# Optimization experiments

Hardware: AMD Instinct MI355X
Metric: run time of the kernel (lower is better)

Reference implementation:

```python
import jax, jax.numpy as jnp
import numpy as np

L, B, D = 1024, 2, 1024
H, DH = 16, 64
DFF = 4096
MEM = 1024
T = L + MEM
SCALE = 1.0 / DH ** 0.5
EPS = 1e-5


def _ln(x, g, b):
    mu = jnp.mean(x, axis=-1, keepdims=True)
    var = jnp.var(x, axis=-1, keepdims=True)
    return (x - mu) * jax.lax.rsqrt(var + EPS) * g + b


def _rel_shift(x):
    # x: [L, T, B, H] -> TXL relative shift
    Lq, Tk = x.shape[0], x.shape[1]
    xp = jnp.pad(x, ((0, 0), (1, 0), (0, 0), (0, 0)))
    xp = xp.reshape(Tk + 1, Lq, *x.shape[2:])
    return xp[1:].reshape(x.shape)


def setup_inputs() -> dict:
    key = jax.random.key(0)
    ks = jax.random.split(key, 16)
    s = 0.02
    inp = {
        "x": jax.random.normal(ks[0], (L, B, D), jnp.float32),
        "pos_emb": jax.random.normal(ks[1], (T, B, D), jnp.float32),
        "pos_bias_u": jax.random.normal(ks[2], (H, DH), jnp.float32) * s,
        "pos_bias_v": jax.random.normal(ks[3], (H, DH), jnp.float32) * s,
        "memory": jax.random.normal(ks[4], (MEM, B, D), jnp.float32),
        "Wq": jax.random.normal(ks[5], (D, H * DH), jnp.float32) * s,
        "Wkv": jax.random.normal(ks[6], (D, 2 * H * DH), jnp.float32) * s,
        "Wo": jax.random.normal(ks[7], (H * DH, D), jnp.float32) * s,
        "Wrel": jax.random.normal(ks[8], (D, H * DH), jnp.float32) * s,
        "ln1_g": jnp.ones((D,), jnp.float32),
        "ln1_b": jnp.zeros((D,), jnp.float32),
        "W1": jax.random.normal(ks[9], (D, DFF), jnp.float32) * s,
        "b1": jnp.zeros((DFF,), jnp.float32),
        "W2": jax.random.normal(ks[10], (DFF, D), jnp.float32) * s,
        "b2": jnp.zeros((D,), jnp.float32),
        "ln2_g": jnp.ones((D,), jnp.float32),
        "ln2_b": jnp.zeros((D,), jnp.float32),
    }
    # causal mask: key position j disallowed if j > i + MEM
    i = jnp.arange(L)[:, None]
    j = jnp.arange(T)[None, :]
    inp["mask"] = jnp.broadcast_to((j > i + MEM)[:, :, None], (L, T, B))
    return inp


def reference(x, pos_emb, pos_bias_u, pos_bias_v, memory, mask,
              Wq, Wkv, Wo, Wrel, ln1_g, ln1_b, W1, b1, W2, b2, ln2_g, ln2_b):
    # --- LearnableMultiheadSelfAttention, vanilla branch (seq_len==1) ---
    c = jnp.concatenate([memory, x], axis=0)                  # [T,B,D]
    kv = c @ Wkv                                              # [T,B,2*H*DH]
    k, v = jnp.split(kv, 2, axis=-1)
    k = k.reshape(T, B, H, DH)
    v = v.reshape(T, B, H, DH)
    r = (pos_emb @ Wrel).reshape(T, B, H, DH)                 # [T,B,H,DH]
    q = (x @ Wq).reshape(L, B, H, DH)                         # [L,B,H,DH]

    AC = jnp.einsum('ibnd,jbnd->ijbn', q + pos_bias_u, k)     # [L,T,B,H]
    BD = jnp.einsum('ibnd,jbnd->ijbn', q + pos_bias_v, r)
    BD = _rel_shift(BD)

    score = (AC + BD) * SCALE
    score = jnp.where(mask[:, :, :, None], -jnp.inf, score)
    prob = jax.nn.softmax(score, axis=1)                      # softmax over keys (dim 1)
    attn_matrix = prob.mean(axis=(2, 3))                      # [L,T]

    vec = jnp.einsum('ijbn,jbnd->ibnd', prob, v)
    attn_out = vec.reshape(L, B, H * DH) @ Wo
    out = _ln(x + attn_out, ln1_g, ln1_b)

    # --- PositionwiseFF ---
    ff = jax.nn.relu(out @ W1 + b1) @ W2 + b2
    out = _ln(out + ff, ln2_g, ln2_b)
    return out, attn_matrix
```

## Files before the change

### kernel.cpp

```cpp
#include <hip/hip_runtime.h>
#include <hip/hip_bf16.h>
#include <hip/hip_fp16.h>

using bf16 = __hip_bfloat16;

#define LQ      1024
#define NBAT    2
#define DMOD    1024
#define NHEAD   16
#define DHEAD   64
#define DFFN    4096
#define MEMLEN  1024
#define TKEY    2048
#define HDIM    1024
#define SCALE_F 0.125f
#define EPS_F   1e-5f
#define NVTILE  392

typedef __attribute__((ext_vector_type(8))) short short8;
typedef __attribute__((ext_vector_type(4))) float f32x4;

__device__ __forceinline__ float ldf(const float* p) { return *p; }
__device__ __forceinline__ float ldf(const bf16* p) { return __bfloat162float(*p); }
__device__ __forceinline__ void stf(float* p, float v) { *p = v; }
__device__ __forceinline__ void stf(bf16* p, float v) { *p = __float2bfloat16(v); }

__device__ __forceinline__ void cpy4(bf16* dst, const float* src) {
    float4 w = *(const float4*)src;
    bf16 t[4] = {__float2bfloat16(w.x), __float2bfloat16(w.y),
                 __float2bfloat16(w.z), __float2bfloat16(w.w)};
    *(uint2*)dst = *(uint2*)t;
}
__device__ __forceinline__ void cpy4(bf16* dst, const bf16* src) {
    *(uint2*)dst = *(const uint2*)src;
}

__device__ __forceinline__ void gload_lds16(const bf16* g, bf16* l) {
    __builtin_amdgcn_global_load_lds(
        (const __attribute__((address_space(1))) unsigned int*)g,
        (__attribute__((address_space(3))) unsigned int*)l, 16, 0, 0);
}

#define SWZ(row, colE) ((row) * 64 + ((colE) ^ (((row) & 7) << 3)))

__global__ __launch_bounds__(256)
void cvt3_bf16_k(const float* __restrict__ s0, bf16* __restrict__ d0, int n0,
                 const float* __restrict__ s1, bf16* __restrict__ d1, int n1,
                 const float* __restrict__ s2, bf16* __restrict__ d2, int n2)
{
    int i = (blockIdx.x * 256 + threadIdx.x) * 8;
    const float* s; bf16* d;
    if (i < n0)           { s = s0; d = d0; }
    else if (i < n0 + n1) { s = s1; d = d1; i -= n0; }
    else if (i < n0 + n1 + n2) { s = s2; d = d2; i -= n0 + n1; }
    else return;
    float4 v0 = *(const float4*)(s + i);
    float4 v1 = *(const float4*)(s + i + 4);
    bf16 t[8] = {__float2bfloat16(v0.x), __float2bfloat16(v0.y),
                 __float2bfloat16(v0.z), __float2bfloat16(v0.w),
                 __float2bfloat16(v1.x), __float2bfloat16(v1.y),
                 __float2bfloat16(v1.z), __float2bfloat16(v1.w)};
    *(uint4*)(d + i) = *(uint4*)t;
}

__device__ __forceinline__ void tcvt_tile(const float* __restrict__ W,
                                          bf16* __restrict__ Wt,
                                          int K, int N, int n0, int k0, int tid,
                                          bf16 (*tile)[65])
{
    const int r = tid >> 2, cb = (tid & 3) * 16;
    #pragma unroll
    for (int e = 0; e < 16; e++)
        tile[r][cb + e] = __float2bfloat16(W[(size_t)(k0 + r) * N + n0 + cb + e]);
    __syncthreads();
    bf16 t[16];
    #pragma unroll
    for (int e = 0; e < 16; e++) t[e] = tile[cb + e][r];
    bf16* dst = Wt + (size_t)(n0 + r) * K + k0 + cb;
    *(uint4*)dst       = ((uint4*)t)[0];
    *(uint4*)(dst + 8) = ((uint4*)t)[1];
}

__global__ __launch_bounds__(256)
void tcvt_bf16_k(const float* __restrict__ W, bf16* __restrict__ Wt, int K, int N)
{
    __shared__ alignas(16) bf16 tile[64][65];
    tcvt_tile(W, Wt, K, N, blockIdx.x * 64, blockIdx.y * 64, threadIdx.x, tile);
}

__global__ __launch_bounds__(256)
void tcvt3_k(const float* __restrict__ Wkv_, bf16* __restrict__ dkv,
             const float* __restrict__ Wrel_, bf16* __restrict__ dr,
             const float* __restrict__ Wq_, bf16* __restrict__ dq)
{
    __shared__ alignas(16) bf16 tile[64][65];
    int bid = blockIdx.x;
    const float* W; bf16* Wt; int N;
    if (bid < 512)      { W = Wkv_;  Wt = dkv; N = 2048; }
    else if (bid < 768) { W = Wrel_; Wt = dr;  N = 1024; bid -= 512; }
    else                { W = Wq_;   Wt = dq;  N = 1024; bid -= 768; }
    const int nb = N / 64;
    tcvt_tile(W, Wt, DMOD, N, (bid % nb) * 64, (bid / nb) * 64, threadIdx.x, tile);
}

template<int SPLITS, bool RELU, typename TOUT>
__device__ __forceinline__ void gemm128_body(
    const bf16* __restrict__ A, const bf16* __restrict__ Bt,
    const float* __restrict__ bias, TOUT* __restrict__ Cbase,
    int M, int N, int K, int bx, int by, int bz,
    bf16* __restrict__ As, bf16* __restrict__ Bs)
{
    const int tid  = threadIdx.x;
    const int wave = tid >> 6, lane = tid & 63;
    const int m0 = by * 128, n0 = bx * 128;
    const int g = lane >> 4, c16 = lane & 15;
    const int wr = (wave >> 1) * 64, wc = (wave & 1) * 64;

    const int klen   = K / SPLITS;
    const int kstart = bz * klen;
    TOUT* C = Cbase + (size_t)bz * M * N;

    f32x4 acc[4][4];
    #pragma unroll
    for (int mi = 0; mi < 4; mi++)
        #pragma unroll
        for (int ni = 0; ni < 4; ni++) acc[mi][ni] = (f32x4)(0.f);

    const int r0 = (wave << 5) + (lane >> 3);
    const int cc = (((lane & 7) ^ (lane >> 3)) << 3);
    const bf16* agp = A  + (size_t)(m0 + r0) * K + kstart + cc;
    const bf16* bgp = Bt + (size_t)(n0 + r0) * K + kstart + cc;
    const int lb = wave * 2048;

    #pragma unroll
    for (int q = 0; q < 4; q++) {
        gload_lds16(agp + (size_t)(q * 8) * K, As + lb + q * 512);
        gload_lds16(bgp + (size_t)(q * 8) * K, Bs + lb + q * 512);
    }

    int cur = 0;
    for (int k0 = 0; k0 < klen; k0 += 64) {
        if (k0 + 64 < klen) {
            #pragma unroll
            for (int q = 0; q < 4; q++) {
                gload_lds16(agp + k0 + 64 + (size_t)(q * 8) * K,
                            As + (cur ^ 1) * 8192 + lb + q * 512);
                gload_lds16(bgp + k0 + 64 + (size_t)(q * 8) * K,
                            Bs + (cur ^ 1) * 8192 + lb + q * 512);
            }
            asm volatile("s_waitcnt vmcnt(8)" ::: "memory");
        } else {
            asm volatile("s_waitcnt vmcnt(0)" ::: "memory");
        }
        __builtin_amdgcn_s_barrier();
        short8 af[4][2], bfr[4][2];
        #pragma unroll
        for (int mi = 0; mi < 4; mi++) {
            const int row = wr + mi * 16 + c16;
            af[mi][0] = *(const short8*)&As[cur * 8192 + SWZ(row, g * 8)];
            af[mi][1] = *(const short8*)&As[cur * 8192 + SWZ(row, 32 + g * 8)];
        }
        #pragma unroll
        for (int ni = 0; ni < 4; ni++) {
            const int row = wc + ni * 16 + c16;
            bfr[ni][0] = *(const short8*)&Bs[cur * 8192 + SWZ(row, g * 8)];
            bfr[ni][1] = *(const short8*)&Bs[cur * 8192 + SWZ(row, 32 + g * 8)];
        }
        #pragma unroll
        for (int mi = 0; mi < 4; mi++)
            #pragma unroll
            for (int ni = 0; ni < 4; ni++) {
                acc[mi][ni] = __builtin_amdgcn_mfma_f32_16x16x32_bf16(
                                  af[mi][0], bfr[ni][0], acc[mi][ni], 0, 0, 0);
                acc[mi][ni] = __builtin_amdgcn_mfma_f32_16x16x32_bf16(
                                  af[mi][1], bfr[ni][1], acc[mi][ni], 0, 0, 0);
            }
        __builtin_amdgcn_s_barrier();
        cur ^= 1;
    }

    const int crow = g * 4;
    #pragma unroll
    for (int ni = 0; ni < 4; ni++) {
        const int n = n0 + wc + ni * 16 + c16;
        const float bv = (SPLITS == 1 && bias) ? bias[n] : 0.f;
        #pragma unroll
        for (int mi = 0; mi < 4; mi++) {
            #pragma unroll
            for (int reg = 0; reg < 4; reg++) {
                const int m = m0 + wr + mi * 16 + crow + reg;
                float v = acc[mi][ni][reg] + bv;
                if (RELU) v = fmaxf(v, 0.f);
                stf(C + (size_t)m * N + n, v);
            }
        }
    }
}

template<int SPLITS, bool RELU, typename TOUT>
__global__ __launch_bounds__(256)
void mgemm128_k(const bf16* __restrict__ A, const bf16* __restrict__ Bt,
                const float* __restrict__ bias, TOUT* __restrict__ Cbase,
                int M, int N, int K)
{
    __shared__ alignas(16) bf16 As[2 * 128 * 64];
    __shared__ alignas(16) bf16 Bs[2 * 128 * 64];
    gemm128_body<SPLITS, RELU, TOUT>(A, Bt, bias, Cbase, M, N, K,
                                     blockIdx.x, blockIdx.y, blockIdx.z, As, Bs);
}

__global__ __launch_bounds__(256)
void proj3_k(const bf16* __restrict__ catc, const bf16* __restrict__ wkvt,
             bf16* __restrict__ kvb,
             const bf16* __restrict__ posc, const bf16* __restrict__ wrelt,
             bf16* __restrict__ rb,
             const bf16* __restrict__ xb, const bf16* __restrict__ wqt,
             float* __restrict__ qb)
{
    __shared__ alignas(16) bf16 As[2 * 128 * 64];
    __shared__ alignas(16) bf16 Bs[2 * 128 * 64];
    int bid = blockIdx.x;
    if (bid < 512) {
        gemm128_body<1, false, bf16>(catc, wkvt, nullptr, kvb,
                                     TKEY * NBAT, 2 * HDIM, DMOD,
                                     bid & 15, bid >> 4, 0, As, Bs);
    } else if (bid < 768) {
        bid -= 512;
        gemm128_body<1, false, bf16>(posc, wrelt, nullptr, rb,
                                     TKEY * NBAT, HDIM, DMOD,
                                     bid & 7, bid >> 3, 0, As, Bs);
    } else {
        bid -= 768;
        gemm128_body<1, false, float>(xb, wqt, nullptr, qb,
                                      LQ * NBAT, HDIM, DMOD,
                                      bid & 7, bid >> 3, 0, As, Bs);
    }
}

template<typename TA, typename TOUT, bool RELU>
__global__ __launch_bounds__(256)
void mgemm64_k(const TA* __restrict__ A0, const TA* __restrict__ A1, int rowsplit,
               const float* __restrict__ Bw, const float* __restrict__ bias,
               TOUT* __restrict__ C, int M, int N, int K)
{
    __shared__ alignas(16) bf16 As[64][72];
    __shared__ alignas(16) bf16 Bs[64][72];
    const int tid  = threadIdx.x;
    const int m0   = blockIdx.y * 64;
    const int n0   = blockIdx.x * 64;
    const int wave = tid >> 6, lane = tid & 63;
    const int g = lane >> 4, c16 = lane & 15;

    f32x4 acc[4];
    #pragma unroll
    for (int nt = 0; nt < 4; nt++) acc[nt] = (f32x4)(0.f);

    const int ar = tid >> 2, akc = (tid & 3) * 16;
    const int grow = m0 + ar;
    const TA* Arow = (grow < rowsplit) ? (A0 + (size_t)grow * K)
                                       : (A1 + (size_t)(grow - rowsplit) * K);
    const int bn = tid & 63, bkb = (tid >> 6) * 16;
    const float* Bcol = Bw + n0 + bn;

    for (int k0 = 0; k0 < K; k0 += 64) {
        cpy4(&As[ar][akc],      Arow + k0 + akc);
        cpy4(&As[ar][akc + 4],  Arow + k0 + akc + 4);
        cpy4(&As[ar][akc + 8],  Arow + k0 + akc + 8);
        cpy4(&As[ar][akc + 12], Arow + k0 + akc + 12);
        {
            bf16 t16[16];
            #pragma unroll
            for (int e = 0; e < 16; e++)
                t16[e] = __float2bfloat16(Bcol[(size_t)(k0 + bkb + e) * N]);
            *(uint4*)&Bs[bn][bkb]     = *(uint4*)&t16[0];
            *(uint4*)&Bs[bn][bkb + 8] = *(uint4*)&t16[8];
        }
        __syncthreads();
        const short8 a0 = *(const short8*)&As[wave * 16 + c16][g * 8];
        const short8 a1 = *(const short8*)&As[wave * 16 + c16][32 + g * 8];
        #pragma unroll
        for (int nt = 0; nt < 4; nt++) {
            acc[nt] = __builtin_amdgcn_mfma_f32_16x16x32_bf16(
                          a0, *(const short8*)&Bs[nt * 16 + c16][g * 8], acc[nt], 0, 0, 0);
            acc[nt] = __builtin_amdgcn_mfma_f32_16x16x32_bf16(
                          a1, *(const short8*)&Bs[nt * 16 + c16][32 + g * 8], acc[nt], 0, 0, 0);
        }
        __syncthreads();
    }

    const int crow = (lane >> 4) * 4, ccol = lane & 15;
    #pragma unroll
    for (int nt = 0; nt < 4; nt++) {
        const int n = n0 + nt * 16 + ccol;
        const float bv = bias ? bias[n] : 0.f;
        #pragma unroll
        for (int rr = 0; rr < 4; rr++) {
            const int m = m0 + wave * 16 + crow + rr;
            float v = acc[nt][rr] + bv;
            if (RELU) v = fmaxf(v, 0.f);
            stf(C + (size_t)m * N + n, v);
        }
    }
}

union Frag8 { bf16 h[8]; short8 v; };

template<bool WRSC>
__global__ __launch_bounds__(256)
void flash_attn_k(const float* __restrict__ q, const bf16* __restrict__ kv,
                  const bf16* __restrict__ rg, const float* __restrict__ ub,
                  const float* __restrict__ vb,
                  float* __restrict__ m_arr, float* __restrict__ l_arr,
                  bf16* __restrict__ vec, __half* __restrict__ scr)
{
    __shared__ alignas(16) bf16 Ks[64][72];
    __shared__ alignas(16) bf16 Rs[128][72];
    __shared__ alignas(16) bf16 Vt[64][72];
    __shared__ alignas(16) bf16 BDs[64][136];

    const int itile = (blockIdx.y < (NBAT * NHEAD / 2))
                          ? blockIdx.x : (gridDim.x - 1 - blockIdx.x);
    const int i0 = itile * 64;
    const int bh = blockIdx.y;
    const int b = bh >> 4, h = bh & 15;
    const int tid = threadIdx.x;
    const int wave = tid >> 6, lane = tid & 63;
    const int g = lane >> 4, c16 = lane & 15;
    const int dib = wave * 16 + g * 4;
    const int tbase = itile * 17 + itile * (itile - 1) / 2;

    Frag8 fu0, fu1, fv0, fv1;
    {
        const float* qrow = q + ((size_t)(i0 + wave * 16 + c16) * NBAT + b) * HDIM + h * DHEAD;
        const float* ubp = ub + h * DHEAD;
        const float* vbp = vb + h * DHEAD;
        #pragma unroll
        for (int e = 0; e < 8; e++) {
            float q0 = qrow[g * 8 + e], q1 = qrow[32 + g * 8 + e];
            fu0.h[e] = __float2bfloat16(q0 + ubp[g * 8 + e]);
            fu1.h[e] = __float2bfloat16(q1 + ubp[32 + g * 8 + e]);
            fv0.h[e] = __float2bfloat16(q0 + vbp[g * 8 + e]);
            fv1.h[e] = __float2bfloat16(q1 + vbp[32 + g * 8 + e]);
        }
    }

    float mrow[4] = {-3e38f, -3e38f, -3e38f, -3e38f};
    float lrow[4] = {0.f, 0.f, 0.f, 0.f};
    f32x4 Oacc[4];
    #pragma unroll
    for (int nt = 0; nt < 4; nt++) Oacc[nt] = (f32x4)(0.f);

    const int ntiles = i0 / 64 + 17;

    for (int t = 0; t < ntiles; t++) {
        const int j0 = t * 64;
        const int jj0 = j0 + (LQ - 64) - i0;
        __half* scp = nullptr;
        if (WRSC) scp = scr + ((size_t)bh * NVTILE + tbase + t) * 4096;
        {
            const int row = tid >> 2, dbase = (tid & 3) * 16;
            const bf16* src = kv + ((size_t)(j0 + row) * NBAT + b) * (2 * HDIM)
                                 + h * DHEAD + dbase;
            *(uint4*)&Ks[row][dbase]     = *(const uint4*)src;
            *(uint4*)&Ks[row][dbase + 8] = *(const uint4*)(src + 8);
        }
        {
            const int row = tid >> 1, dbase = (tid & 1) * 32;
            const int jj = jj0 + row;
            if (jj < TKEY) {
                const bf16* src = rg + ((size_t)jj * NBAT + b) * HDIM + h * DHEAD + dbase;
                #pragma unroll
                for (int u = 0; u < 4; u++)
                    *(uint4*)&Rs[row][dbase + u * 8] = *(const uint4*)(src + u * 8);
            } else {
                const uint4 z = make_uint4(0, 0, 0, 0);
                #pragma unroll
                for (int u = 0; u < 4; u++)
                    *(uint4*)&Rs[row][dbase + u * 8] = z;
            }
        }
        {
            const int j = tid & 63, dbase = (tid >> 6) * 16;
            const bf16* src = kv + ((size_t)(j0 + j) * NBAT + b) * (2 * HDIM)
                                 + HDIM + h * DHEAD + dbase;
            bf16 tmp[16];
            *(uint4*)&tmp[0] = *(const uint4*)src;
            *(uint4*)&tmp[8] = *(const uint4*)(src + 8);
            #pragma unroll
            for (int e = 0; e < 16; e++) Vt[dbase + e][j] = tmp[e];
        }
        __syncthreads();
        f32x4 ac[4];
        #pragma unroll
        for (int nt = 0; nt < 4; nt++) {
            ac[nt] = (f32x4)(0.f);
            ac[nt] = __builtin_amdgcn_mfma_f32_16x16x32_bf16(
                         fu0.v, *(const short8*)&Ks[nt * 16 + c16][g * 8], ac[nt], 0, 0, 0);
            ac[nt] = __builtin_amdgcn_mfma_f32_16x16x32_bf16(
                         fu1.v, *(const short8*)&Ks[nt * 16 + c16][32 + g * 8], ac[nt], 0, 0, 0);
        }
        #pragma unroll
        for (int nt = 0; nt < 8; nt++) {
            f32x4 bd = (f32x4)(0.f);
            bd = __builtin_amdgcn_mfma_f32_16x16x32_bf16(
                     fv0.v, *(const short8*)&Rs[nt * 16 + c16][g * 8], bd, 0, 0, 0);
            bd = __builtin_amdgcn_mfma_f32_16x16x32_bf16(
                     fv1.v, *(const short8*)&Rs[nt * 16 + c16][32 + g * 8], bd, 0, 0, 0);
            #pragma unroll
            for (int reg = 0; reg < 4; reg++)
                BDs[dib + reg][nt * 16 + c16] = __float2bfloat16(bd[reg]);
        }
        float sv[4][4];
        #pragma unroll
        for (int reg = 0; reg < 4; reg++) {
            const int di = dib + reg;
            const int colbase = 63 - di;
            __half hv[4];
            #pragma unroll
            for (int nt = 0; nt < 4; nt++) {
                const int dj = nt * 16 + c16;
                float s = (ac[nt][reg] +
                           __bfloat162float(BDs[di][colbase + dj])) * SCALE_F;
                if (j0 + dj > i0 + di + MEMLEN) s = -1e30f;
                sv[nt][reg] = s;
                if (WRSC) hv[nt] = __float2half(s);
            }
            if (WRSC) *(uint2*)&scp[di * 64 + c16 * 4] = *(uint2*)hv;
        }
        #pragma unroll
        for (int reg = 0; reg < 4; reg++) {
            float tm = fmaxf(fmaxf(sv[0][reg], sv[1][reg]),
                             fmaxf(sv[2][reg], sv[3][reg]));
            #pragma unroll
            for (int mk = 1; mk < 16; mk <<= 1)
                tm = fmaxf(tm, __shfl_xor(tm, mk));
            const float nm = fmaxf(mrow[reg], tm);
            const float alpha = __expf(mrow[reg] - nm);
            float ev[4];
            #pragma unroll
            for (int nt = 0; nt < 4; nt++) ev[nt] = __expf(sv[nt][reg] - nm);
            float ps = ev[0] + ev[1] + ev[2] + ev[3];
            #pragma unroll
            for (int mk = 1; mk < 16; mk <<= 1)
                ps += __shfl_xor(ps, mk);
            lrow[reg] = lrow[reg] * alpha + ps;
            mrow[reg] = nm;
            #pragma unroll
            for (int nt = 0; nt < 4; nt++) {
                Oacc[nt][reg] *= alpha;
                BDs[dib + reg][nt * 16 + c16] = __float2bfloat16(ev[nt]);
            }
        }
        short8 p0 = *(const short8*)&BDs[wave * 16 + c16][g * 8];
        short8 p1 = *(const short8*)&BDs[wave * 16 + c16][32 + g * 8];
        #pragma unroll
        for (int nt = 0; nt < 4; nt++) {
            Oacc[nt] = __builtin_amdgcn_mfma_f32_16x16x32_bf16(
                           p0, *(const short8*)&Vt[nt * 16 + c16][g * 8], Oacc[nt], 0, 0, 0);
            Oacc[nt] = __builtin_amdgcn_mfma_f32_16x16x32_bf16(
                           p1, *(const short8*)&Vt[nt * 16 + c16][32 + g * 8], Oacc[nt], 0, 0, 0);
        }
        __syncthreads();
    }

    float invl[4];
    #pragma unroll
    for (int reg = 0; reg < 4; reg++) invl[reg] = 1.f / lrow[reg];
    #pragma unroll
    for (int nt = 0; nt < 4; nt++)
        #pragma unroll
        for (int reg = 0; reg < 4; reg++)
            vec[((size_t)(i0 + dib + reg) * NBAT + b) * HDIM + h * DHEAD + nt * 16 + c16]
                = __float2bfloat16(Oacc[nt][reg] * invl[reg]);
    if (c16 == 0) {
        #pragma unroll
        for (int reg = 0; reg < 4; reg++) {
            const int idx = ((i0 + dib + reg) * NBAT + b) * NHEAD + h;
            m_arr[idx] = mrow[reg];
            l_arr[idx] = lrow[reg];
        }
    }
}

__global__ __launch_bounds__(256)
void attn_sum2_k(const __half* __restrict__ scr, const float* __restrict__ m_arr,
                 const float* __restrict__ l_arr, float* __restrict__ attn)
{
    int f = blockIdx.x, it = 0, base = 0;
    for (it = 0; it < 16; it++) {
        const int cnt = it + 17;
        if (f < base + cnt) break;
        base += cnt;
    }
    const int i0 = it * 64;
    const int j0 = (f - base) * 64;
    const int tid = threadIdx.x;
    const int row = blockIdx.y * 32 + (tid >> 3);
    const int pb = (tid & 7) * 8;
    const int i = i0 + row;

    float acc[8] = {0.f, 0.f, 0.f, 0.f, 0.f, 0.f, 0.f, 0.f};

    for (int bh = 0; bh < NBAT * NHEAD; bh++) {
        const int b = bh >> 4, h = bh & 15;
        const __half* sp = scr + ((size_t)bh * NVTILE + blockIdx.x) * 4096 + row * 64 + pb;
        const int idx = (i * NBAT + b) * NHEAD + h;
        const float mi = m_arr[idx];
        const float il = 1.f / l_arr[idx];
        union { uint4 v; __half hx[8]; } u;
        u.v = *(const uint4*)sp;
        #pragma unroll
        for (int e = 0; e < 8; e++)
            acc[e] += __expf(__half2float(u.hx[e]) - mi) * il;
    }
    const float inv = 1.f / (NBAT * NHEAD);
    #pragma unroll
    for (int e = 0; e < 8; e++) {
        const int p = pb + e;
        const int j = (p & 3) * 16 + (p >> 2);
        attn[(size_t)i * TKEY + j0 + j] = acc[e] * inv;
    }
}

__global__ __launch_bounds__(256)
void attn_mat4_k(const float* __restrict__ q, const bf16* __restrict__ kv,
                 const bf16* __restrict__ rg, const float* __restrict__ ub,
                 const float* __restrict__ vb, const float* __restrict__ m_arr,
                 const float* __restrict__ l_arr, float* __restrict__ attn)
{
    int f = blockIdx.x, it = 0, base = 0;
    for (it = 0; it < 16; it++) {
        const int cnt = it + 17;
        if (f < base + cnt) break;
        base += cnt;
    }
    const int i0 = it * 64;
    const int j0 = (f - base) * 64;
    const int bhb = blockIdx.y * 16;

    __shared__ alignas(16) bf16 Ks[64][72];
    __shared__ alignas(16) bf16 Rs[128][72];
    __shared__ alignas(16) bf16 BDs[64][136];
    const int tid = threadIdx.x;
    const int wave = tid >> 6, lane = tid & 63;
    const int g = lane >> 4, c16 = lane & 15;
    const int dib = wave * 16 + g * 4;
    const int jj0 = j0 + (LQ - 64) - i0;
    float psum[4][4] = {};

    for (int bh = bhb; bh < bhb + 16; bh++) {
        const int b = bh >> 4, h = bh & 15;
        Frag8 fu0, fu1, fv0, fv1;
        {
            const float* qrow = q + ((size_t)(i0 + wave * 16 + c16) * NBAT + b) * HDIM + h * DHEAD;
            const float* ubp = ub + h * DHEAD;
            const float* vbp = vb + h * DHEAD;
            #pragma unroll
            for (int e = 0; e < 8; e++) {
                float q0 = qrow[g * 8 + e], q1 = qrow[32 + g * 8 + e];
                fu0.h[e] = __float2bfloat16(q0 + ubp[g * 8 + e]);
                fu1.h[e] = __float2bfloat16(q1 + ubp[32 + g * 8 + e]);
                fv0.h[e] = __float2bfloat16(q0 + vbp[g * 8 + e]);
                fv1.h[e] = __float2bfloat16(q1 + vbp[32 + g * 8 + e]);
            }
        }
        {
            const int row = tid >> 2, dbase = (tid & 3) * 16;
            const bf16* src = kv + ((size_t)(j0 + row) * NBAT + b) * (2 * HDIM)
                                 + h * DHEAD + dbase;
            *(uint4*)&Ks[row][dbase]     = *(const uint4*)src;
            *(uint4*)&Ks[row][dbase + 8] = *(const uint4*)(src + 8);
        }
        {
            const int row = tid >> 1, dbase = (tid & 1) * 32;
            const int jj = jj0 + row;
            if (jj < TKEY) {
                const bf16* src = rg + ((size_t)jj * NBAT + b) * HDIM + h * DHEAD + dbase;
                #pragma unroll
                for (int u = 0; u < 4; u++)
                    *(uint4*)&Rs[row][dbase + u * 8] = *(const uint4*)(src + u * 8);
            } else {
                const uint4 z = make_uint4(0, 0, 0, 0);
                #pragma unroll
                for (int u = 0; u < 4; u++)
                    *(uint4*)&Rs[row][dbase + u * 8] = z;
            }
        }
        __syncthreads();
        f32x4 ac[4];
        #pragma unroll
        for (int nt = 0; nt < 4; nt++) {
            ac[nt] = (f32x4)(0.f);
            ac[nt] = __builtin_amdgcn_mfma_f32_16x16x32_bf16(
                         fu0.v, *(const short8*)&Ks[nt * 16 + c16][g * 8], ac[nt], 0, 0, 0);
            ac[nt] = __builtin_amdgcn_mfma_f32_16x16x32_bf16(
                         fu1.v, *(const short8*)&Ks[nt * 16 + c16][32 + g * 8], ac[nt], 0, 0, 0);
        }
        #pragma unroll
        for (int nt = 0; nt < 8; nt++) {
            f32x4 bd = (f32x4)(0.f);
            bd = __builtin_amdgcn_mfma_f32_16x16x32_bf16(
                     fv0.v, *(const short8*)&Rs[nt * 16 + c16][g * 8], bd, 0, 0, 0);
            bd = __builtin_amdgcn_mfma_f32_16x16x32_bf16(
                     fv1.v, *(const short8*)&Rs[nt * 16 + c16][32 + g * 8], bd, 0, 0, 0);
            #pragma unroll
            for (int reg = 0; reg < 4; reg++)
                BDs[dib + reg][nt * 16 + c16] = __float2bfloat16(bd[reg]);
        }
        #pragma unroll
        for (int reg = 0; reg < 4; reg++) {
            const int di = dib + reg;
            const int colbase = 63 - di;
            const int idx = ((i0 + di) * NBAT + b) * NHEAD + h;
            const float mi = m_arr[idx];
            const float il = 1.f / l_arr[idx];
            #pragma unroll
            for (int nt = 0; nt < 4; nt++) {
                const int dj = nt * 16 + c16;
                float s = (ac[nt][reg] +
                           __bfloat162float(BDs[di][colbase + dj])) * SCALE_F;
                float p = (j0 + dj > i0 + di + MEMLEN) ? 0.f : __expf(s - mi) * il;
                psum[nt][reg] += p;
            }
        }
        __syncthreads();
    }
    const float inv = 1.f / (NBAT * NHEAD);
    #pragma unroll
    for (int nt = 0; nt < 4; nt++)
        #pragma unroll
        for (int reg = 0; reg < 4; reg++)
            atomicAdd(&attn[(size_t)(i0 + dib + reg) * TKEY + j0 + nt * 16 + c16],
                      psum[nt][reg] * inv);
}

template<typename T1, typename T2, typename TOUT>
__global__ __launch_bounds__(256)
void ln_k(const T1* __restrict__ a, const T2* __restrict__ c,
          const float* __restrict__ g, const float* __restrict__ bb,
          TOUT* __restrict__ out)
{
    const int row = blockIdx.x;
    const int tid = threadIdx.x;
    const size_t base = (size_t)row * DMOD;
    float vals[4];
    float s = 0.f, sq = 0.f;
    #pragma unroll
    for (int t = 0; t < 4; t++) {
        const int dcol = tid + t * 256;
        float v = ldf(a + base + dcol) + ldf(c + base + dcol);
        vals[t] = v; s += v; sq += v * v;
    }
    __shared__ float rs[256], rq[256];
    rs[tid] = s; rq[tid] = sq;
    __syncthreads();
    for (int st = 128; st > 0; st >>= 1) {
        if (tid < st) { rs[tid] += rs[tid + st]; rq[tid] += rq[tid + st]; }
        __syncthreads();
    }
    const float mean = rs[0] / DMOD;
    const float var = rq[0] / DMOD - mean * mean;
    const float rstd = rsqrtf(fmaxf(var, 0.f) + EPS_F);
    #pragma unroll
    for (int t = 0; t < 4; t++) {
        const int dcol = tid + t * 256;
        float v = (vals[t] - mean) * rstd * g[dcol] + bb[dcol];
        stf(out + base + dcol, v);
    }
}

template<typename TA, int NP, bool HASB, typename TOUT>
__global__ __launch_bounds__(256)
void lnp_k(const TA* __restrict__ a, const float* __restrict__ part, size_t pstride,
           const float* __restrict__ biasvec, const float* __restrict__ g,
           const float* __restrict__ bb, TOUT* __restrict__ out)
{
    const int row = blockIdx.x;
    const int tid = threadIdx.x;
    const size_t base = (size_t)row * DMOD;
    float vals[4];
    float s = 0.f, sq = 0.f;
    #pragma unroll
    for (int t = 0; t < 4; t++) {
        const int dcol = tid + t * 256;
        float v = ldf(a + base + dcol);
        #pragma unroll
        for (int p = 0; p < NP; p++) v += part[(size_t)p * pstride + base + dcol];
        if (HASB) v += biasvec[dcol];
        vals[t] = v; s += v; sq += v * v;
    }
    __shared__ float rs[256], rq[256];
    rs[tid] = s; rq[tid] = sq;
    __syncthreads();
    for (int st = 128; st > 0; st >>= 1) {
        if (tid < st) { rs[tid] += rs[tid + st]; rq[tid] += rq[tid + st]; }
        __syncthreads();
    }
    const float mean = rs[0] / DMOD;
    const float var = rq[0] / DMOD - mean * mean;
    const float rstd = rsqrtf(fmaxf(var, 0.f) + EPS_F);
    #pragma unroll
    for (int t = 0; t < 4; t++) {
        const int dcol = tid + t * 256;
        float v = (vals[t] - mean) * rstd * g[dcol] + bb[dcol];
        stf(out + base + dcol, v);
    }
}

__global__ void fill_zero_k(float* __restrict__ p, int n) {
    int i = blockIdx.x * 256 + threadIdx.x;
    if (i < n) p[i] = 0.f;
}

extern "C" void kernel_launch(void* const* d_in, const int* in_sizes, int n_in,
                              void* d_out, int out_size, void* d_ws, size_t ws_size,
                              hipStream_t stream)
{
    const float* x    = (const float*)d_in[0];
    const float* pos  = (const float*)d_in[1];
    const float* ub   = (const float*)d_in[2];
    const float* vb   = (const float*)d_in[3];
    const float* memp = (const float*)d_in[4];
    const float* Wq   = (const float*)d_in[5];
    const float* Wkv  = (const float*)d_in[6];
    const float* Wo   = (const float*)d_in[7];
    const float* Wrel = (const float*)d_in[8];
    const float* ln1g = (const float*)d_in[9];
    const float* ln1b = (const float*)d_in[10];
    const float* W1   = (const float*)d_in[11];
    const float* b1   = (const float*)d_in[12];
    const float* W2   = (const float*)d_in[13];
    const float* b2   = (const float*)d_in[14];
    const float* ln2g = (const float*)d_in[15];
    const float* ln2b = (const float*)d_in[16];

    char* wsb = (char*)d_ws;
    const size_t MB = 1048576;
    bf16*  kvb   = (bf16*)(wsb + 0);
    bf16*  h1    = (bf16*)(wsb + 0);
    bf16*  rb    = (bf16*)(wsb + 16 * MB);
    bf16*  aout  = (bf16*)(wsb + 16 * MB);
    bf16*  f2o   = (bf16*)(wsb + 16 * MB);
    bf16*  out1  = (bf16*)(wsb + 20 * MB);
    bf16*  vecb  = (bf16*)(wsb + 24 * MB);
    float* m_arr = (float*)(wsb + 28 * MB);
    float* l_arr = (float*)(wsb + 28 * MB + 131072);
    const size_t ws_need_old = 28 * MB + 262144;
    bf16*  catc  = (bf16*)(wsb + 30 * MB);
    bf16*  posc  = (bf16*)(wsb + 38 * MB);
    float* part2 = (float*)(wsb + 30 * MB);
    bf16*  wscr  = (bf16*)(wsb + 46 * MB);
    const size_t ws_need_new = 54 * MB;
    __half* scrh = (__half*)(wsb + 54 * MB);
    const size_t ws_need_sc = 54 * MB + (size_t)NVTILE * 32 * 4096 * 2;

    float* outp  = (float*)d_out;
    float* attnp = outp + (size_t)LQ * NBAT * DMOD;
    float* qb    = outp;

    const dim3 blk(256);
    const size_t PSTRIDE = (size_t)LQ * NBAT * DMOD;
    const int NATTN = LQ * TKEY;

    if (ws_size < ws_need_old) {
        fill_zero_k<<<dim3((out_size + 255) / 256), blk, 0, stream>>>(outp, out_size);
        return;
    }

    if (ws_size >= ws_need_new) {
        const bool useSC = (ws_size >= ws_need_sc);
        const int nCat = MEMLEN * NBAT * DMOD;
        const int nPos = TKEY * NBAT * DMOD;
        cvt3_bf16_k<<<dim3((2 * nCat + nPos) / 2048), blk, 0, stream>>>(
            memp, catc, nCat, x, catc + (size_t)nCat, nCat, pos, posc, nPos);
        tcvt3_k<<<dim3(1024), blk, 0, stream>>>(
            Wkv, wscr, Wrel, wscr + (size_t)2 * MB, Wq, wscr + (size_t)3 * MB);

        proj3_k<<<dim3(896), blk, 0, stream>>>(
            catc, wscr, kvb,
            posc, wscr + (size_t)2 * MB, rb,
            catc + (size_t)nCat, wscr + (size_t)3 * MB, qb);

        fill_zero_k<<<dim3((NATTN + 255) / 256), blk, 0, stream>>>(attnp, NATTN);

        if (useSC) {
            flash_attn_k<true><<<dim3(LQ / 64, NBAT * NHEAD), blk, 0, stream>>>(
                qb, kvb, rb, ub, vb, m_arr, l_arr, vecb, scrh);
            attn_sum2_k<<<dim3(NVTILE, 2), blk, 0, stream>>>(scrh, m_arr, l_arr, attnp);
        } else {
            flash_attn_k<false><<<dim3(LQ / 64, NBAT * NHEAD), blk, 0, stream>>>(
                qb, kvb, rb, ub, vb, m_arr, l_arr, vecb, nullptr);
            attn_mat4_k<<<dim3(NVTILE, 2), blk, 0, stream>>>(
                qb, kvb, rb, ub, vb, m_arr, l_arr, attnp);
        }

        tcvt_bf16_k<<<dim3(DMOD / 64, HDIM / 64), blk, 0, stream>>>(Wo, wscr, HDIM, DMOD);
        mgemm128_k<2, false, float><<<dim3(DMOD / 128, LQ * NBAT / 128, 2), blk, 0, stream>>>(
            vecb, wscr, nullptr, part2, LQ * NBAT, DMOD, HDIM);
        lnp_k<float, 2, false, bf16><<<dim3(LQ * NBAT), blk, 0, stream>>>(
            x, part2, PSTRIDE, nullptr, ln1g, ln1b, out1);
        tcvt_bf16_k<<<dim3(DFFN / 64, DMOD / 64), blk, 0, stream>>>(W1, wscr, DMOD, DFFN);
        mgemm128_k<1, true, bf16><<<dim3(DFFN / 128, LQ * NBAT / 128, 1), blk, 0, stream>>>(
            out1, wscr, b1, h1, LQ * NBAT, DFFN, DMOD);
        tcvt_bf16_k<<<dim3(DMOD / 64, DFFN / 64), blk, 0, stream>>>(W2, wscr, DFFN, DMOD);
        mgemm128_k<2, false, float><<<dim3(DMOD / 128, LQ * NBAT / 128, 2), blk, 0, stream>>>(
            h1, wscr, nullptr, part2, LQ * NBAT, DMOD, DFFN);
        lnp_k<bf16, 2, true, float><<<dim3(LQ * NBAT), blk, 0, stream>>>(
            out1, part2, PSTRIDE, b2, ln2g, ln2b, outp);
        return;
    }

    mgemm64_k<float, bf16, false><<<dim3(2 * HDIM / 64, TKEY * NBAT / 64), blk, 0, stream>>>(
        memp, x, MEMLEN * NBAT, Wkv, nullptr, kvb, TKEY * NBAT, 2 * HDIM, DMOD);
    mgemm64_k<float, bf16, false><<<dim3(HDIM / 64, TKEY * NBAT / 64), blk, 0, stream>>>(
        pos, pos, TKEY * NBAT, Wrel, nullptr, rb, TKEY * NBAT, HDIM, DMOD);
    mgemm64_k<float, float, false><<<dim3(HDIM / 64, LQ * NBAT / 64), blk, 0, stream>>>(
        x, x, LQ * NBAT, Wq, nullptr, qb, LQ * NBAT, HDIM, DMOD);

    fill_zero_k<<<dim3((NATTN + 255) / 256), blk, 0, stream>>>(attnp, NATTN);
    flash_attn_k<false><<<dim3(LQ / 64, NBAT * NHEAD), blk, 0, stream>>>(
        qb, kvb, rb, ub, vb, m_arr, l_arr, vecb, nullptr);
    attn_mat4_k<<<dim3(NVTILE, 2), blk, 0, stream>>>(
        qb, kvb, rb, ub, vb, m_arr, l_arr, attnp);

    mgemm64_k<bf16, bf16, false><<<dim3(DMOD / 64, LQ * NBAT / 64), blk, 0, stream>>>(
        vecb, vecb, LQ * NBAT, Wo, nullptr, aout, LQ * NBAT, DMOD, HDIM);
    ln_k<float, bf16, bf16><<<dim3(LQ * NBAT), blk, 0, stream>>>(x, aout, ln1g, ln1b, out1);
    mgemm64_k<bf16, bf16, true><<<dim3(DFFN / 64, LQ * NBAT / 64), blk, 0, stream>>>(
        out1, out1, LQ * NBAT, W1, b1, h1, LQ * NBAT, DFFN, DMOD);
    mgemm64_k<bf16, bf16, false><<<dim3(DMOD / 64, LQ * NBAT / 64), blk, 0, stream>>>(
        h1, h1, LQ * NBAT, W2, b2, f2o, LQ * NBAT, DMOD, DFFN);
    ln_k<bf16, bf16, float><<<dim3(LQ * NBAT), blk, 0, stream>>>(out1, f2o, ln2g, ln2b, outp);
}
```

Measured before the change: 437.9 us.

## Add 256x256-tile 8-wave MFMA GEMM for projections and FFN with split-K 4

Introduces a 256x256 output tile GEMM body using 512 threads (8 waves, each computing 128x64), double-buffered LDS staging with interleaved A/B prefetch and priority hints. It replaces the 128-tile kernels for the fused Q/KV/Rel projection, Wo, W1 and W2 GEMMs on the scratch-enabled path, and raises split-K for Wo/W2 from 2 to 4 with a new partial buffer and matching layernorm reduction. The goal is higher arithmetic intensity and fewer global loads per FLOP. The cost is far fewer blocks (e.g. 224 for projections, 64 per Wo/W2 split-K launch), which may leave many of the CUs idle, plus more partial-sum traffic.

```diff
diff --git a/kernel.cpp b/kernel.cpp
--- a/kernel.cpp
+++ b/kernel.cpp
@@ -101,6 +101,199 @@
     else                { W = Wq_;   Wt = dq;  N = 1024; bid -= 768; }
     const int nb = N / 64;
     tcvt_tile(W, Wt, DMOD, N, (bid % nb) * 64, (bid / nb) * 64, threadIdx.x, tile);
+}
+
+template<int SPLITS, bool RELU, typename TOUT>
+__device__ __forceinline__ void gemm256_body(
+    const bf16* __restrict__ A, const bf16* __restrict__ Bt,
+    const float* __restrict__ bias, TOUT* __restrict__ Cbase,
+    int M, int N, int K, int bx, int by, int bz,
+    bf16* __restrict__ As, bf16* __restrict__ Bs)
+{
+    const int tid = threadIdx.x;
+    const int wid = tid >> 6, lane = tid & 63;
+    const int wm = wid >> 2, wn = wid & 3;
+    const int g = lane >> 4, c16 = lane & 15;
+    const int m0 = by * 256, n0 = bx * 256;
+    const int klen = K / SPLITS, kstart = bz * klen;
+    const int NT = klen / 64;
+    TOUT* C = Cbase + (size_t)bz * M * N;
+
+    f32x4 acc[8][4];
+    #pragma unroll
+    for (int mi = 0; mi < 8; mi++)
+        #pragma unroll
+        for (int ni = 0; ni < 4; ni++) acc[mi][ni] = (f32x4)(0.f);
+
+    const int srow = wid * 16 + (lane >> 3);
+    const int cc   = (((lane & 7) ^ (lane >> 3)) << 3);
+    const bf16* ag = A  + (size_t)(m0 + srow) * K + kstart + cc;
+    const bf16* bg = Bt + (size_t)(n0 + srow) * K + kstart + cc;
+    const int lwb = wid * 1024;
+
+    auto stageA = [&](int nb, int kt) {
+        #pragma unroll
+        for (int ha = 0; ha < 2; ha++)
+            #pragma unroll
+            for (int q = 0; q < 2; q++)
+                gload_lds16(ag + (size_t)(ha * 128 + q * 8) * K + (size_t)kt * 64,
+                            As + nb * 16384 + ha * 8192 + lwb + q * 512);
+    };
+    auto stageB = [&](int nb, int kt) {
+        #pragma unroll
+        for (int hb = 0; hb < 2; hb++)
+            #pragma unroll
+            for (int q = 0; q < 2; q++)
+                gload_lds16(bg + (size_t)(hb * 128 + q * 8) * K + (size_t)kt * 64,
+                            Bs + nb * 16384 + hb * 8192 + lwb + q * 512);
+    };
+    const int arb = wm * 8192;
+    const int brb = (wn >> 1) * 8192;
+    const int brow = (wn & 1) * 64;
+
+    stageA(0, 0); stageB(0, 0);
+    asm volatile("s_waitcnt vmcnt(0)" ::: "memory");
+    __builtin_amdgcn_s_barrier();
+
+    for (int t = 0; t < NT; t++) {
+        const int b = t & 1, nb = b ^ 1;
+        const bool pf = (t + 1 < NT);
+        short8 af[4][2], bf_[2][2];
+        if (pf) stageA(nb, t + 1);
+        #pragma unroll
+        for (int mi = 0; mi < 4; mi++)
+            #pragma unroll
+            for (int kk = 0; kk < 2; kk++)
+                af[mi][kk] = *(const short8*)&As[b * 16384 + arb +
+                                 SWZ(mi * 16 + c16, kk * 32 + g * 8)];
+        #pragma unroll
+        for (int ni = 0; ni < 2; ni++)
+            #pragma unroll
+            for (int kk = 0; kk < 2; kk++)
+                bf_[ni][kk] = *(const short8*)&Bs[b * 16384 + brb +
+                                 SWZ(brow + ni * 16 + c16, kk * 32 + g * 8)];
+        __builtin_amdgcn_s_setprio(1);
+        #pragma unroll
+        for (int mi = 0; mi < 4; mi++)
+            #pragma unroll
+            for (int ni = 0; ni < 2; ni++)
+                #pragma unroll
+                for (int kk = 0; kk < 2; kk++)
+                    acc[mi][ni] = __builtin_amdgcn_mfma_f32_16x16x32_bf16(
+                                      af[mi][kk], bf_[ni][kk], acc[mi][ni], 0, 0, 0);
+        __builtin_amdgcn_s_setprio(0);
+        __builtin_amdgcn_s_barrier();
+        if (pf) stageB(nb, t + 1);
+        #pragma unroll
+        for (int ni = 0; ni < 2; ni++)
+            #pragma unroll
+            for (int kk = 0; kk < 2; kk++)
+                bf_[ni][kk] = *(const short8*)&Bs[b * 16384 + brb +
+                                 SWZ(brow + (ni + 2) * 16 + c16, kk * 32 + g * 8)];
+        __builtin_amdgcn_s_setprio(1);
+        #pragma unroll
+        for (int mi = 0; mi < 4; mi++)
+            #pragma unroll
+            for (int ni = 0; ni < 2; ni++)
+                #pragma unroll
+                for (int kk = 0; kk < 2; kk++)
+                    acc[mi][ni + 2] = __builtin_amdgcn_mfma_f32_16x16x32_bf16(
+                                      af[mi][kk], bf_[ni][kk], acc[mi][ni + 2], 0, 0, 0);
+        __builtin_amdgcn_s_setprio(0);
+        __builtin_amdgcn_s_barrier();
+        #pragma unroll
+        for (int mi = 0; mi < 4; mi++)
+            #pragma unroll
+            for (int kk = 0; kk < 2; kk++)
+                af[mi][kk] = *(const short8*)&As[b * 16384 + arb +
+                                 SWZ((mi + 4) * 16 + c16, kk * 32 + g * 8)];
+        __builtin_amdgcn_s_setprio(1);
+        #pragma unroll
+        for (int mi = 0; mi < 4; mi++)
+            #pragma unroll
+            for (int ni = 0; ni < 2; ni++)
+                #pragma unroll
+                for (int kk = 0; kk < 2; kk++)
+                    acc[mi + 4][ni + 2] = __builtin_amdgcn_mfma_f32_16x16x32_bf16(
+                                      af[mi][kk], bf_[ni][kk], acc[mi + 4][ni + 2], 0, 0, 0);
+        __builtin_amdgcn_s_setprio(0);
+        __builtin_amdgcn_s_barrier();
+        #pragma unroll
+        for (int ni = 0; ni < 2; ni++)
+            #pragma unroll
+            for (int kk = 0; kk < 2; kk++)
+                bf_[ni][kk] = *(const short8*)&Bs[b * 16384 + brb +
+                                 SWZ(brow + ni * 16 + c16, kk * 32 + g * 8)];
+        __builtin_amdgcn_s_setprio(1);
+        #pragma unroll
+        for (int mi = 0; mi < 4; mi++)
+            #pragma unroll
+            for (int ni = 0; ni < 2; ni++)
+                #pragma unroll
+                for (int kk = 0; kk < 2; kk++)
+                    acc[mi + 4][ni] = __builtin_amdgcn_mfma_f32_16x16x32_bf16(
+                                      af[mi][kk], bf_[ni][kk], acc[mi + 4][ni], 0, 0, 0);
+        __builtin_amdgcn_s_setprio(0);
+        if (pf) asm volatile("s_waitcnt vmcnt(0)" ::: "memory");
+        __builtin_amdgcn_s_barrier();
+    }
+
+    const int crow = g * 4;
+    #pragma unroll
+    for (int ni = 0; ni < 4; ni++) {
+        const int n = n0 + wn * 64 + ni * 16 + c16;
+        const float bv = (SPLITS == 1 && bias) ? bias[n] : 0.f;
+        #pragma unroll
+        for (int mi = 0; mi < 8; mi++) {
+            #pragma unroll
+            for (int reg = 0; reg < 4; reg++) {
+                const int m = m0 + wm * 128 + mi * 16 + crow + reg;
+                float v = acc[mi][ni][reg] + bv;
+                if (RELU) v = fmaxf(v, 0.f);
+                stf(C + (size_t)m * N + n, v);
+            }
+        }
+    }
+}
+
+template<int SPLITS, bool RELU, typename TOUT>
+__global__ __launch_bounds__(512)
+void mgemm256_k(const bf16* __restrict__ A, const bf16* __restrict__ Bt,
+                const float* __restrict__ bias, TOUT* __restrict__ Cbase,
+                int M, int N, int K)
+{
+    __shared__ alignas(16) bf16 As[2 * 2 * 8192];
+    __shared__ alignas(16) bf16 Bs[2 * 2 * 8192];
+    gemm256_body<SPLITS, RELU, TOUT>(A, Bt, bias, Cbase, M, N, K,
+                                     blockIdx.x, blockIdx.y, blockIdx.z, As, Bs);
+}
+
+__global__ __launch_bounds__(512)
+void proj3_256_k(const bf16* __restrict__ catc, const bf16* __restrict__ wkvt,
+                 bf16* __restrict__ kvb,
+                 const bf16* __restrict__ posc, const bf16* __restrict__ wrelt,
+                 bf16* __restrict__ rb,
+                 const bf16* __restrict__ xb, const bf16* __restrict__ wqt,
+                 float* __restrict__ qb)
+{
+    __shared__ alignas(16) bf16 As[2 * 2 * 8192];
+    __shared__ alignas(16) bf16 Bs[2 * 2 * 8192];
+    int bid = blockIdx.x;
+    if (bid < 128) {
+        gemm256_body<1, false, bf16>(catc, wkvt, nullptr, kvb,
+                                     TKEY * NBAT, 2 * HDIM, DMOD,
+                                     bid & 7, bid >> 3, 0, As, Bs);
+    } else if (bid < 192) {
+        bid -= 128;
+        gemm256_body<1, false, bf16>(posc, wrelt, nullptr, rb,
+                                     TKEY * NBAT, HDIM, DMOD,
+                                     bid & 3, bid >> 2, 0, As, Bs);
+    } else {
+        bid -= 192;
+        gemm256_body<1, false, float>(xb, wqt, nullptr, qb,
+                                      LQ * NBAT, HDIM, DMOD,
+                                      bid & 3, bid >> 2, 0, As, Bs);
+    }
 }
 
 template<int SPLITS, bool RELU, typename TOUT>
@@ -752,6 +945,7 @@
     bf16*  wscr  = (bf16*)(wsb + 46 * MB);
     const size_t ws_need_new = 54 * MB;
     __half* scrh = (__half*)(wsb + 54 * MB);
+    float* part4 = (float*)(wsb + 54 * MB);
     const size_t ws_need_sc = 54 * MB + (size_t)NVTILE * 32 * 4096 * 2;
 
     float* outp  = (float*)d_out;
@@ -759,6 +953,7 @@
     float* qb    = outp;
 
     const dim3 blk(256);
+    const dim3 blk2(512);
     const size_t PSTRIDE = (size_t)LQ * NBAT * DMOD;
     const int NATTN = LQ * TKEY;
 
@@ -776,37 +971,56 @@
         tcvt3_k<<<dim3(1024), blk, 0, stream>>>(
             Wkv, wscr, Wrel, wscr + (size_t)2 * MB, Wq, wscr + (size_t)3 * MB);
 
-        proj3_k<<<dim3(896), blk, 0, stream>>>(
-            catc, wscr, kvb,
-            posc, wscr + (size_t)2 * MB, rb,
-            catc + (size_t)nCat, wscr + (size_t)3 * MB, qb);
-
-        fill_zero_k<<<dim3((NATTN + 255) / 256), blk, 0, stream>>>(attnp, NATTN);
-
         if (useSC) {
+            proj3_256_k<<<dim3(224), blk2, 0, stream>>>(
+                catc, wscr, kvb,
+                posc, wscr + (size_t)2 * MB, rb,
+                catc + (size_t)nCat, wscr + (size_t)3 * MB, qb);
+
+            fill_zero_k<<<dim3((NATTN + 255) / 256), blk, 0, stream>>>(attnp, NATTN);
             flash_attn_k<true><<<dim3(LQ / 64, NBAT * NHEAD), blk, 0, stream>>>(
                 qb, kvb, rb, ub, vb, m_arr, l_arr, vecb, scrh);
             attn_sum2_k<<<dim3(NVTILE, 2), blk, 0, stream>>>(scrh, m_arr, l_arr, attnp);
+
+            tcvt_bf16_k<<<dim3(DMOD / 64, HDIM / 64), blk, 0, stream>>>(Wo, wscr, HDIM, DMOD);
+            mgemm256_k<4, false, float><<<dim3(DMOD / 256, LQ * NBAT / 256, 4), blk2, 0, stream>>>(
+                vecb, wscr, nullptr, part4, LQ * NBAT, DMOD, HDIM);
+            lnp_k<float, 4, false, bf16><<<dim3(LQ * NBAT), blk, 0, stream>>>(
+                x, part4, PSTRIDE, nullptr, ln1g, ln1b, out1);
+            tcvt_bf16_k<<<dim3(DFFN / 64, DMOD / 64), blk, 0, stream>>>(W1, wscr, DMOD, DFFN);
+            mgemm256_k<1, true, bf16><<<dim3(DFFN / 256, LQ * NBAT / 256, 1), blk2, 0, stream>>>(
+                out1, wscr, b1, h1, LQ * NBAT, DFFN, DMOD);
+            tcvt_bf16_k<<<dim3(DMOD / 64, DFFN / 64), blk, 0, stream>>>(W2, wscr, DFFN, DMOD);
+            mgemm256_k<4, false, float><<<dim3(DMOD / 256, LQ * NBAT / 256, 4), blk2, 0, stream>>>(
+                h1, wscr, nullptr, part4, LQ * NBAT, DMOD, DFFN);
+            lnp_k<bf16, 4, true, float><<<dim3(LQ * NBAT), blk, 0, stream>>>(
+                out1, part4, PSTRIDE, b2, ln2g, ln2b, outp);
         } else {
+            proj3_k<<<dim3(896), blk, 0, stream>>>(
+                catc, wscr, kvb,
+                posc, wscr + (size_t)2 * MB, rb,
+                catc + (size_t)nCat, wscr + (size_t)3 * MB, qb);
+
+            fill_zero_k<<<dim3((NATTN + 255) / 256), blk, 0, stream>>>(attnp, NATTN);
             flash_attn_k<false><<<dim3(LQ / 64, NBAT * NHEAD), blk, 0, stream>>>(
                 qb, kvb, rb, ub, vb, m_arr, l_arr, vecb, nullptr);
             attn_mat4_k<<<dim3(NVTILE, 2), blk, 0, stream>>>(
                 qb, kvb, rb, ub, vb, m_arr, l_arr, attnp);
-        }
-
-        tcvt_bf16_k<<<dim3(DMOD / 64, HDIM / 64), blk, 0, stream>>>(Wo, wscr, HDIM, DMOD);
-        mgemm128_k<2, false, float><<<dim3(DMOD / 128, LQ * NBAT / 128, 2), blk, 0, stream>>>(
-            vecb, wscr, nullptr, part2, LQ * NBAT, DMOD, HDIM);
-        lnp_k<float, 2, false, bf16><<<dim3(LQ * NBAT), blk, 0, stream>>>(
-            x, part2, PSTRIDE, nullptr, ln1g, ln1b, out1);
-        tcvt_bf16_k<<<dim3(DFFN / 64, DMOD / 64), blk, 0, stream>>>(W1, wscr, DMOD, DFFN);
-        mgemm128_k<1, true, bf16><<<dim3(DFFN / 128, LQ * NBAT / 128, 1), blk, 0, stream>>>(
-            out1, wscr, b1, h1, LQ * NBAT, DFFN, DMOD);
-        tcvt_bf16_k<<<dim3(DMOD / 64, DFFN / 64), blk, 0, stream>>>(W2, wscr, DFFN, DMOD);
-        mgemm128_k<2, false, float><<<dim3(DMOD / 128, LQ * NBAT / 128, 2), blk, 0, stream>>>(
-            h1, wscr, nullptr, part2, LQ * NBAT, DMOD, DFFN);
-        lnp_k<bf16, 2, true, float><<<dim3(LQ * NBAT), blk, 0, stream>>>(
-            out1, part2, PSTRIDE, b2, ln2g, ln2b, outp);
+
+            tcvt_bf16_k<<<dim3(DMOD / 64, HDIM / 64), blk, 0, stream>>>(Wo, wscr, HDIM, DMOD);
+            mgemm128_k<2, false, float><<<dim3(DMOD / 128, LQ * NBAT / 128, 2), blk, 0, stream>>>(
+                vecb, wscr, nullptr, part2, LQ * NBAT, DMOD, HDIM);
+            lnp_k<float, 2, false, bf16><<<dim3(LQ * NBAT), blk, 0, stream>>>(
+                x, part2, PSTRIDE, nullptr, ln1g, ln1b, out1);
+            tcvt_bf16_k<<<dim3(DFFN / 64, DMOD / 64), blk, 0, stream>>>(W1, wscr, DMOD, DFFN);
+            mgemm128_k<1, true, bf16><<<dim3(DFFN / 128, LQ * NBAT / 128, 1), blk, 0, stream>>>(
+                out1, wscr, b1, h1, LQ * NBAT, DFFN, DMOD);
+            tcvt_bf16_k<<<dim3(DMOD / 64, DFFN / 64), blk, 0, stream>>>(W2, wscr, DFFN, DMOD);
+            mgemm128_k<2, false, float><<<dim3(DMOD / 128, LQ * NBAT / 128, 2), blk, 0, stream>>>(
+                h1, wscr, nullptr, part2, LQ * NBAT, DMOD, DFFN);
+            lnp_k<bf16, 2, true, float><<<dim3(LQ * NBAT), blk, 0, stream>>>(
+                out1, part2, PSTRIDE, b2, ln2g, ln2b, outp);
+        }
         return;
     }
 
```

New measurement: 483.5 us. 10.4% more time.

## Prefetch next K/R/V tile into registers and fold zero-fill into attn sum

Applied to the files above, without the earlier changes.

The flash attention loop now issues the global loads for the next K, R and V tile into registers during the softmax of the current tile. It writes them to shared memory after the barrier, which hides global-load latency behind compute. Separately, attn_sum2_k now covers the full 32x16 tile grid and writes zeros for masked tiles itself, so the separate fill_zero pass over the attention matrix is dropped on the scratch path. The cost is extra registers for the prefetch buffers, which may lower occupancy, plus an extra barrier per iteration.

```diff
diff --git a/kernel.cpp b/kernel.cpp
--- a/kernel.cpp
+++ b/kernel.cpp
@@ -329,6 +329,52 @@
     const int dib = wave * 16 + g * 4;
     const int tbase = itile * 17 + itile * (itile - 1) / 2;
 
+    const int krow = tid >> 2, kd = (tid & 3) * 16;
+    const int rrow = tid >> 1, rd = (tid & 1) * 32;
+    const int vj   = tid & 63, vd = (tid >> 6) * 16;
+
+    uint4 kr[2], rr[4], vr[2];
+
+    auto load_tile = [&](int t) {
+        const int j0n = t * 64;
+        const int jj0n = j0n + (LQ - 64) - i0;
+        {
+            const bf16* src = kv + ((size_t)(j0n + krow) * NBAT + b) * (2 * HDIM)
+                                 + h * DHEAD + kd;
+            kr[0] = *(const uint4*)src;
+            kr[1] = *(const uint4*)(src + 8);
+        }
+        {
+            const int jj = jj0n + rrow;
+            if (jj < TKEY) {
+                const bf16* src = rg + ((size_t)jj * NBAT + b) * HDIM + h * DHEAD + rd;
+                #pragma unroll
+                for (int u = 0; u < 4; u++) rr[u] = *(const uint4*)(src + u * 8);
+            } else {
+                const uint4 z = make_uint4(0, 0, 0, 0);
+                #pragma unroll
+                for (int u = 0; u < 4; u++) rr[u] = z;
+            }
+        }
+        {
+            const bf16* src = kv + ((size_t)(j0n + vj) * NBAT + b) * (2 * HDIM)
+                                 + HDIM + h * DHEAD + vd;
+            vr[0] = *(const uint4*)src;
+            vr[1] = *(const uint4*)(src + 8);
+        }
+    };
+    auto write_tile = [&]() {
+        *(uint4*)&Ks[krow][kd]     = kr[0];
+        *(uint4*)&Ks[krow][kd + 8] = kr[1];
+        #pragma unroll
+        for (int u = 0; u < 4; u++) *(uint4*)&Rs[rrow][rd + u * 8] = rr[u];
+        bf16 tmp[16];
+        *(uint4*)&tmp[0] = vr[0];
+        *(uint4*)&tmp[8] = vr[1];
+        #pragma unroll
+        for (int e = 0; e < 16; e++) Vt[vd + e][vj] = tmp[e];
+    };
+
     Frag8 fu0, fu1, fv0, fv1;
     {
         const float* qrow = q + ((size_t)(i0 + wave * 16 + c16) * NBAT + b) * HDIM + h * DHEAD;
@@ -352,44 +398,14 @@
 
     const int ntiles = i0 / 64 + 17;
 
+    load_tile(0);
+    write_tile();
+    __syncthreads();
+
     for (int t = 0; t < ntiles; t++) {
         const int j0 = t * 64;
-        const int jj0 = j0 + (LQ - 64) - i0;
         __half* scp = nullptr;
         if (WRSC) scp = scr + ((size_t)bh * NVTILE + tbase + t) * 4096;
-        {
-            const int row = tid >> 2, dbase = (tid & 3) * 16;
-            const bf16* src = kv + ((size_t)(j0 + row) * NBAT + b) * (2 * HDIM)
-                                 + h * DHEAD + dbase;
-            *(uint4*)&Ks[row][dbase]     = *(const uint4*)src;
-            *(uint4*)&Ks[row][dbase + 8] = *(const uint4*)(src + 8);
-        }
-        {
-            const int row = tid >> 1, dbase = (tid & 1) * 32;
-            const int jj = jj0 + row;
-            if (jj < TKEY) {
-                const bf16* src = rg + ((size_t)jj * NBAT + b) * HDIM + h * DHEAD + dbase;
-                #pragma unroll
-                for (int u = 0; u < 4; u++)
-                    *(uint4*)&Rs[row][dbase + u * 8] = *(const uint4*)(src + u * 8);
-            } else {
-                const uint4 z = make_uint4(0, 0, 0, 0);
-                #pragma unroll
-                for (int u = 0; u < 4; u++)
-                    *(uint4*)&Rs[row][dbase + u * 8] = z;
-            }
-        }
-        {
-            const int j = tid & 63, dbase = (tid >> 6) * 16;
-            const bf16* src = kv + ((size_t)(j0 + j) * NBAT + b) * (2 * HDIM)
-                                 + HDIM + h * DHEAD + dbase;
-            bf16 tmp[16];
-            *(uint4*)&tmp[0] = *(const uint4*)src;
-            *(uint4*)&tmp[8] = *(const uint4*)(src + 8);
-            #pragma unroll
-            for (int e = 0; e < 16; e++) Vt[dbase + e][j] = tmp[e];
-        }
-        __syncthreads();
         f32x4 ac[4];
         #pragma unroll
         for (int nt = 0; nt < 4; nt++) {
@@ -427,6 +443,7 @@
             }
             if (WRSC) *(uint2*)&scp[di * 64 + c16 * 4] = *(uint2*)hv;
         }
+        if (t + 1 < ntiles) load_tile(t + 1);
         #pragma unroll
         for (int reg = 0; reg < 4; reg++) {
             float tm = fmaxf(fmaxf(sv[0][reg], sv[1][reg]),
@@ -461,6 +478,10 @@
                            p1, *(const short8*)&Vt[nt * 16 + c16][32 + g * 8], Oacc[nt], 0, 0, 0);
         }
         __syncthreads();
+        if (t + 1 < ntiles) {
+            write_tile();
+            __syncthreads();
+        }
     }
 
     float invl[4];
@@ -486,24 +507,28 @@
 void attn_sum2_k(const __half* __restrict__ scr, const float* __restrict__ m_arr,
                  const float* __restrict__ l_arr, float* __restrict__ attn)
 {
-    int f = blockIdx.x, it = 0, base = 0;
-    for (it = 0; it < 16; it++) {
-        const int cnt = it + 17;
-        if (f < base + cnt) break;
-        base += cnt;
-    }
-    const int i0 = it * 64;
-    const int j0 = (f - base) * 64;
+    const int it = blockIdx.x >> 5, jt = blockIdx.x & 31;
+    const int i0 = it * 64, j0 = jt * 64;
     const int tid = threadIdx.x;
     const int row = blockIdx.y * 32 + (tid >> 3);
     const int pb = (tid & 7) * 8;
     const int i = i0 + row;
 
+    if (jt > it + 16) {
+        #pragma unroll
+        for (int e = 0; e < 8; e++) {
+            const int p = pb + e;
+            const int j = (p & 3) * 16 + (p >> 2);
+            attn[(size_t)i * TKEY + j0 + j] = 0.f;
+        }
+        return;
+    }
+    const int ft = it * 17 + it * (it - 1) / 2 + jt;
+
     float acc[8] = {0.f, 0.f, 0.f, 0.f, 0.f, 0.f, 0.f, 0.f};
-
     for (int bh = 0; bh < NBAT * NHEAD; bh++) {
         const int b = bh >> 4, h = bh & 15;
-        const __half* sp = scr + ((size_t)bh * NVTILE + blockIdx.x) * 4096 + row * 64 + pb;
+        const __half* sp = scr + ((size_t)bh * NVTILE + ft) * 4096 + row * 64 + pb;
         const int idx = (i * NBAT + b) * NHEAD + h;
         const float mi = m_arr[idx];
         const float il = 1.f / l_arr[idx];
@@ -781,13 +806,12 @@
             posc, wscr + (size_t)2 * MB, rb,
             catc + (size_t)nCat, wscr + (size_t)3 * MB, qb);
 
-        fill_zero_k<<<dim3((NATTN + 255) / 256), blk, 0, stream>>>(attnp, NATTN);
-
         if (useSC) {
             flash_attn_k<true><<<dim3(LQ / 64, NBAT * NHEAD), blk, 0, stream>>>(
                 qb, kvb, rb, ub, vb, m_arr, l_arr, vecb, scrh);
-            attn_sum2_k<<<dim3(NVTILE, 2), blk, 0, stream>>>(scrh, m_arr, l_arr, attnp);
+            attn_sum2_k<<<dim3(512, 2), blk, 0, stream>>>(scrh, m_arr, l_arr, attnp);
         } else {
+            fill_zero_k<<<dim3((NATTN + 255) / 256), blk, 0, stream>>>(attnp, NATTN);
             flash_attn_k<false><<<dim3(LQ / 64, NBAT * NHEAD), blk, 0, stream>>>(
                 qb, kvb, rb, ub, vb, m_arr, l_arr, vecb, nullptr);
             attn_mat4_k<<<dim3(NVTILE, 2), blk, 0, stream>>>(
```

Result: slower. 447.0 us (+2.1%).
